# Optimization experiments

Hardware: AMD Instinct MI355X
Metric: run time of the kernel (lower is better)

The kernel has to match this reference:

```python
import jax, jax.numpy as jnp
import numpy as np

B, T, C, H = 4, 2048, 1024, 16
D = C // H  # head_dim = 64

def setup_inputs() -> dict:
    key = jax.random.key(0)
    k1, k2, k3 = jax.random.split(key, 3)
    x = jax.random.normal(k1, (B, T, C), dtype=jnp.float32)
    W_attn = jax.random.normal(k2, (C, 3 * C), dtype=jnp.float32) * (C ** -0.5)
    b_attn = jnp.zeros((3 * C,), dtype=jnp.float32)
    W_proj = jax.random.normal(k3, (C, C), dtype=jnp.float32) * (C ** -0.5)
    b_proj = jnp.zeros((C,), dtype=jnp.float32)
    return {"x": x, "W_attn": W_attn, "b_attn": b_attn, "W_proj": W_proj, "b_proj": b_proj}

def reference(x, W_attn, b_attn, W_proj, b_proj):
    Bc, Tc, Cc = x.shape
    qkv = x @ W_attn + b_attn                       # [B,T,3C]
    q, k, v = jnp.split(qkv, 3, axis=-1)
    q = q.reshape(Bc, Tc, H, D).transpose(0, 2, 1, 3)  # [B,H,T,D]
    k = k.reshape(Bc, Tc, H, D).transpose(0, 2, 1, 3)
    v = v.reshape(Bc, Tc, H, D).transpose(0, 2, 1, 3)
    scores = jnp.einsum('bhqd,bhkd->bhqk', q, k) / jnp.sqrt(jnp.float32(D))
    causal = jnp.tril(jnp.ones((Tc, Tc), dtype=bool))
    scores = jnp.where(causal[None, None, :, :], scores, jnp.float32(-jnp.inf))
    wei = jax.nn.softmax(scores, axis=-1)           # dropout=0 -> identity
    out = jnp.einsum('bhqk,bhkd->bhqd', wei, v)     # [B,H,T,D]
    out = out.transpose(0, 2, 1, 3).reshape(Bc, Tc, Cc)
    return out @ W_proj + b_proj
```

## Files before the change

kernel.cpp:

```cpp
#include <hip/hip_runtime.h>
#include <cstdint>
#include <cstddef>

#define Bsz   4
#define Tsz   2048
#define Csz   1024
#define Hn    16
#define Dh    64
#define Mrows 8192
#define KD    1024

#define NEG_BIG (-1.0e30f)
#define SCL2  0.18033688011112042f
#define PBIAS (-11.541560327111707f)

typedef unsigned short u16;
typedef __bf16  bf16x8 __attribute__((ext_vector_type(8)));
typedef __bf16  bf16x2 __attribute__((ext_vector_type(2)));
typedef float   f32x4  __attribute__((ext_vector_type(4)));
typedef unsigned int u32x4 __attribute__((ext_vector_type(4)));

__device__ __forceinline__ u16 f2bf(float f) {
  union { float f; unsigned int i; } v; v.f = f;
  unsigned int u = v.i;
  return (u16)((u + 0x7fffu + ((u >> 16) & 1u)) >> 16);
}
__device__ __forceinline__ unsigned int pack2bf(float a, float b) {
#if __has_builtin(__builtin_amdgcn_cvt_pk_bf16_f32)
  union { bf16x2 h; unsigned int u; } cv;
  cv.h = __builtin_amdgcn_cvt_pk_bf16_f32(a, b);
  return cv.u;
#else
  return (unsigned int)f2bf(a) | ((unsigned int)f2bf(b) << 16);
#endif
}
__device__ __forceinline__ unsigned int pack2bf_trunc(float lo, float hi) {
  return __builtin_amdgcn_perm(__builtin_bit_cast(unsigned int, hi),
                               __builtin_bit_cast(unsigned int, lo),
                               0x07060302u);
}
__device__ __forceinline__ float fast_exp2(float x) {
#if __has_builtin(__builtin_amdgcn_exp2f)
  return __builtin_amdgcn_exp2f(x);
#else
  return exp2f(x);
#endif
}

__global__ __launch_bounds__(256)
void cvt_f32_bf16(const float* __restrict__ in, u16* __restrict__ out, int n4) {
  const int i = blockIdx.x * 256 + threadIdx.x;
  if (i >= n4) return;
  const float4 v = ((const float4*)in)[i];
  uint2 o;
  o.x = pack2bf(v.x, v.y);
  o.y = pack2bf(v.z, v.w);
  ((uint2*)out)[i] = o;
}

__global__ __launch_bounds__(256)
void transpose_f32_bf16(const float* __restrict__ in, u16* __restrict__ out,
                        int rows, int cols) {
  __shared__ u16 tile[64][65];
  const int tc = blockIdx.x * 64, tr = blockIdx.y * 64;
  const int x = threadIdx.x & 63, y0 = threadIdx.x >> 6;
#pragma unroll
  for (int yy = 0; yy < 64; yy += 4) {
    int r = yy + y0;
    tile[r][x] = f2bf(in[(size_t)(tr + r) * cols + tc + x]);
  }
  __syncthreads();
#pragma unroll
  for (int yy = 0; yy < 64; yy += 4) {
    int r = yy + y0;
    out[(size_t)(tc + r) * rows + tr + x] = tile[x][r];
  }
}

template<int MODE>
__global__ __launch_bounds__(256)
void gemm_bt(const u16* __restrict__ A, const u16* __restrict__ BT,
             const float* __restrict__ bias, u16* __restrict__ o0,
             u16* __restrict__ o1, u16* __restrict__ o2,
             float* __restrict__ fout, int N) {
  __shared__ u16 lsA[128 * 32];
  __shared__ u16 lsB[128 * 32];
  const int tid  = threadIdx.x;
  const int lane = tid & 63;
  const int wid  = tid >> 6;
  const int wm   = wid & 1, wn = wid >> 1;
  const int quad = lane >> 4, l15 = lane & 15;
  const int m0 = blockIdx.y * 128, n0 = blockIdx.x * 128;

  f32x4 acc[4][4];
#pragma unroll
  for (int i = 0; i < 4; ++i)
#pragma unroll
    for (int j = 0; j < 4; ++j) acc[i][j] = (f32x4){0.f, 0.f, 0.f, 0.f};

#if __has_builtin(__builtin_amdgcn_global_load_lds)
  const int srow = lane >> 2, schunk = lane & 3;
  const u16* gA = A  + (size_t)(m0 + wid * 32 + srow) * KD + schunk * 8;
  const u16* gB = BT + (size_t)(n0 + wid * 32 + srow) * KD + schunk * 8;
  u16* lA0 = &lsA[(wid * 32) * 32];
  u16* lB0 = &lsB[(wid * 32) * 32];
#endif

  for (int kk = 0; kk < KD; kk += 32) {
#if __has_builtin(__builtin_amdgcn_global_load_lds)
#pragma unroll
    for (int i = 0; i < 2; ++i) {
      __builtin_amdgcn_global_load_lds(
          (const __attribute__((address_space(1))) void*)(gA + (size_t)i * 16 * KD + kk),
          (__attribute__((address_space(3))) void*)(lA0 + i * 16 * 32), 16, 0, 0);
      __builtin_amdgcn_global_load_lds(
          (const __attribute__((address_space(1))) void*)(gB + (size_t)i * 16 * KD + kk),
          (__attribute__((address_space(3))) void*)(lB0 + i * 16 * 32), 16, 0, 0);
    }
#else
#pragma unroll
    for (int cc = 0; cc < 2; ++cc) {
      int c = tid + cc * 256;
      int row = c >> 2, ch = c & 3;
      *(uint4*)&lsA[row * 32 + ch * 8] =
          *(const uint4*)&A[(size_t)(m0 + row) * KD + kk + ch * 8];
      *(uint4*)&lsB[row * 32 + ch * 8] =
          *(const uint4*)&BT[(size_t)(n0 + row) * KD + kk + ch * 8];
    }
#endif
    __syncthreads();
    bf16x8 af[4], bfv[4];
#pragma unroll
    for (int i = 0; i < 4; ++i)
      af[i] = *(const bf16x8*)&lsA[(wm * 64 + i * 16 + l15) * 32 + quad * 8];
#pragma unroll
    for (int j = 0; j < 4; ++j)
      bfv[j] = *(const bf16x8*)&lsB[(wn * 64 + j * 16 + l15) * 32 + quad * 8];
#pragma unroll
    for (int i = 0; i < 4; ++i)
#pragma unroll
      for (int j = 0; j < 4; ++j)
        acc[i][j] = __builtin_amdgcn_mfma_f32_16x16x32_bf16(af[i], bfv[j],
                                                            acc[i][j], 0, 0, 0);
    __syncthreads();
  }

#pragma unroll
  for (int i = 0; i < 4; ++i) {
#pragma unroll
    for (int j = 0; j < 4; ++j) {
      const int colb = n0 + wn * 64 + j * 16 + l15;
      const float bv = bias[colb];
      float vals[4];
#pragma unroll
      for (int r = 0; r < 4; ++r) vals[r] = acc[i][j][r] + bv;
      const int row0 = m0 + wm * 64 + i * 16 + quad * 4;
      if (MODE == 0) {
        const int b = row0 >> 11, t0 = row0 & (Tsz - 1);
        const int region = colb >> 10;
        const int nc = colb & (Csz - 1);
        const int h = nc >> 6, d = nc & 63;
        if (region == 2) {
          uint2 st;
          st.x = pack2bf(vals[0], vals[1]);
          st.y = pack2bf(vals[2], vals[3]);
          *(uint2*)&o2[((size_t)((b << 4) + h) * Dh + d) * Tsz + t0] = st;
        } else {
          u16* dst = (region == 0) ? o0 : o1;
#pragma unroll
          for (int r = 0; r < 4; ++r)
            dst[(size_t)(((b << 4) + h) * Tsz + t0 + r) * Dh + d] = f2bf(vals[r]);
        }
      } else {
#pragma unroll
        for (int r = 0; r < 4; ++r)
          fout[(size_t)(row0 + r) * N + colb] = vals[r];
      }
    }
  }
}

__global__ __launch_bounds__(128, 4)
void attn_fused(const u16* __restrict__ qb, const u16* __restrict__ kbuf,
                const u16* __restrict__ vT, u16* __restrict__ outp) {
  __shared__ u16 Kl[64 * 72];
  __shared__ u16 Vt[64 * 72];
  const int tid = threadIdx.x, lane = tid & 63, w = tid >> 6;
  const int quad = lane >> 4, l15 = lane & 15;
  const int bh = blockIdx.x;
  const int jq = 31 - blockIdx.y;
  const int b = bh >> 4, h = bh & 15;
  const u16* Q   = qb   + (size_t)bh * Tsz * Dh;
  const u16* Kg  = kbuf + (size_t)bh * Tsz * Dh;
  const u16* VTg = vT   + (size_t)bh * Dh * Tsz;

  const int qrowA = jq * 64 + w * 32 + l15;
  const int qrowB = qrowA + 16;
  const bf16x8 bqA0 = *(const bf16x8*)&Q[(size_t)qrowA * Dh + quad * 8];
  const bf16x8 bqA1 = *(const bf16x8*)&Q[(size_t)qrowA * Dh + 32 + quad * 8];
  const bf16x8 bqB0 = *(const bf16x8*)&Q[(size_t)qrowB * Dh + quad * 8];
  const bf16x8 bqB1 = *(const bf16x8*)&Q[(size_t)qrowB * Dh + 32 + quad * 8];

  f32x4 OA[4], OB[4];
#pragma unroll
  for (int nb = 0; nb < 4; ++nb) {
    OA[nb] = (f32x4){0.f, 0.f, 0.f, 0.f};
    OB[nb] = (f32x4){0.f, 0.f, 0.f, 0.f};
  }
  float lA = 0.f, lB = 0.f;

  for (int j = 0; j <= jq; ++j) {
    const int kb = j * 64;
#pragma unroll
    for (int cc = 0; cc < 4; ++cc) {
      const int c = tid + cc * 128;
      const int rr = c >> 3, off = c & 7;
      *(uint4*)&Kl[rr * 72 + off * 8] =
          *(const uint4*)&Kg[(size_t)(kb + rr) * Dh + off * 8];
      const uint4 vv = *(const uint4*)&VTg[(size_t)rr * Tsz + kb + off * 8];
      const int g0 = off * 2, g1 = off * 2 + 1;
      uint2 st0; st0.x = vv.x; st0.y = vv.y;
      uint2 st1; st1.x = vv.z; st1.y = vv.w;
      *(uint2*)&Vt[rr * 72 + ((g0 >> 3) * 32 + (g0 & 3) * 8 + ((g0 >> 2) & 1) * 4)] = st0;
      *(uint2*)&Vt[rr * 72 + ((g1 >> 3) * 32 + (g1 & 3) * 8 + ((g1 >> 2) & 1) * 4)] = st1;
    }
    __syncthreads();

    const bool diag = (j == jq);
    const int tmaxA = diag ? (2 * w + 1) : 4;
    const int tmaxB = diag ? (2 * w + 2) : 4;

    f32x4 SA[4], SB[4];
#pragma unroll
    for (int t = 0; t < 4; ++t) {
      SA[t] = (f32x4){0.f, 0.f, 0.f, 0.f};
      SB[t] = (f32x4){0.f, 0.f, 0.f, 0.f};
    }
#pragma unroll
    for (int t = 0; t < 4; ++t) {
      if (t < tmaxB) {
        const bf16x8 ak0 = *(const bf16x8*)&Kl[(t * 16 + l15) * 72 + quad * 8];
        const bf16x8 ak1 = *(const bf16x8*)&Kl[(t * 16 + l15) * 72 + 32 + quad * 8];
        if (t < tmaxA) {
          SA[t] = __builtin_amdgcn_mfma_f32_16x16x32_bf16(ak0, bqA0, SA[t], 0, 0, 0);
          SA[t] = __builtin_amdgcn_mfma_f32_16x16x32_bf16(ak1, bqA1, SA[t], 0, 0, 0);
        }
        SB[t] = __builtin_amdgcn_mfma_f32_16x16x32_bf16(ak0, bqB0, SB[t], 0, 0, 0);
        SB[t] = __builtin_amdgcn_mfma_f32_16x16x32_bf16(ak1, bqB1, SB[t], 0, 0, 0);
      }
    }

    float pA[4][4], pB[4][4];
    if (diag) {
#pragma unroll
      for (int t = 0; t < 4; ++t) {
        const int key0 = kb + t * 16 + quad * 4;
#pragma unroll
        for (int r = 0; r < 4; ++r) {
          if (t < tmaxA) {
            const float sv = (key0 + r <= qrowA) ? SA[t][r] : NEG_BIG;
            pA[t][r] = fast_exp2(__builtin_fmaf(sv, SCL2, PBIAS));
            lA += pA[t][r];
          } else pA[t][r] = 0.f;
          if (t < tmaxB) {
            const float sv = (key0 + r <= qrowB) ? SB[t][r] : NEG_BIG;
            pB[t][r] = fast_exp2(__builtin_fmaf(sv, SCL2, PBIAS));
            lB += pB[t][r];
          } else pB[t][r] = 0.f;
        }
      }
    } else {
#pragma unroll
      for (int t = 0; t < 4; ++t)
#pragma unroll
        for (int r = 0; r < 4; ++r) {
          pA[t][r] = fast_exp2(__builtin_fmaf(SA[t][r], SCL2, PBIAS));
          lA += pA[t][r];
          pB[t][r] = fast_exp2(__builtin_fmaf(SB[t][r], SCL2, PBIAS));
          lB += pB[t][r];
        }
    }

    {
      u32x4 puA, puB;
      puA[0] = pack2bf_trunc(pA[0][0], pA[0][1]);
      puA[1] = pack2bf_trunc(pA[0][2], pA[0][3]);
      puA[2] = pack2bf_trunc(pA[1][0], pA[1][1]);
      puA[3] = pack2bf_trunc(pA[1][2], pA[1][3]);
      puB[0] = pack2bf_trunc(pB[0][0], pB[0][1]);
      puB[1] = pack2bf_trunc(pB[0][2], pB[0][3]);
      puB[2] = pack2bf_trunc(pB[1][0], pB[1][1]);
      puB[3] = pack2bf_trunc(pB[1][2], pB[1][3]);
      const bf16x8 pbA = __builtin_bit_cast(bf16x8, puA);
      const bf16x8 pbB = __builtin_bit_cast(bf16x8, puB);
#pragma unroll
      for (int nb = 0; nb < 4; ++nb) {
        const bf16x8 av = *(const bf16x8*)&Vt[(nb * 16 + l15) * 72 + quad * 8];
        OA[nb] = __builtin_amdgcn_mfma_f32_16x16x32_bf16(av, pbA, OA[nb], 0, 0, 0);
        OB[nb] = __builtin_amdgcn_mfma_f32_16x16x32_bf16(av, pbB, OB[nb], 0, 0, 0);
      }
    }
    if (tmaxB > 2) {
      u32x4 puA, puB;
      puA[0] = pack2bf_trunc(pA[2][0], pA[2][1]);
      puA[1] = pack2bf_trunc(pA[2][2], pA[2][3]);
      puA[2] = pack2bf_trunc(pA[3][0], pA[3][1]);
      puA[3] = pack2bf_trunc(pA[3][2], pA[3][3]);
      puB[0] = pack2bf_trunc(pB[2][0], pB[2][1]);
      puB[1] = pack2bf_trunc(pB[2][2], pB[2][3]);
      puB[2] = pack2bf_trunc(pB[3][0], pB[3][1]);
      puB[3] = pack2bf_trunc(pB[3][2], pB[3][3]);
      const bf16x8 pbA = __builtin_bit_cast(bf16x8, puA);
      const bf16x8 pbB = __builtin_bit_cast(bf16x8, puB);
#pragma unroll
      for (int nb = 0; nb < 4; ++nb) {
        const bf16x8 av = *(const bf16x8*)&Vt[(nb * 16 + l15) * 72 + 32 + quad * 8];
        OA[nb] = __builtin_amdgcn_mfma_f32_16x16x32_bf16(av, pbA, OA[nb], 0, 0, 0);
        OB[nb] = __builtin_amdgcn_mfma_f32_16x16x32_bf16(av, pbB, OB[nb], 0, 0, 0);
      }
    }
    __syncthreads();
  }

  float ltA = lA + __shfl_xor(lA, 16, 64);
  ltA += __shfl_xor(ltA, 32, 64);
  float ltB = lB + __shfl_xor(lB, 16, 64);
  ltB += __shfl_xor(ltB, 32, 64);
  const float invA = 1.0f / ltA, invB = 1.0f / ltB;
#pragma unroll
  for (int nb = 0; nb < 4; ++nb) {
    uint2 st;
    st.x = pack2bf(OA[nb][0] * invA, OA[nb][1] * invA);
    st.y = pack2bf(OA[nb][2] * invA, OA[nb][3] * invA);
    *(uint2*)&outp[(size_t)(b * Tsz + qrowA) * Csz + h * Dh + nb * 16 + quad * 4] = st;
    st.x = pack2bf(OB[nb][0] * invB, OB[nb][1] * invB);
    st.y = pack2bf(OB[nb][2] * invB, OB[nb][3] * invB);
    *(uint2*)&outp[(size_t)(b * Tsz + qrowB) * Csz + h * Dh + nb * 16 + quad * 4] = st;
  }
}

extern "C" void kernel_launch(void* const* d_in, const int* in_sizes, int n_in,
                              void* d_out, int out_size, void* d_ws, size_t ws_size,
                              hipStream_t stream) {
  const float* x      = (const float*)d_in[0];
  const float* W_attn = (const float*)d_in[1];
  const float* b_attn = (const float*)d_in[2];
  const float* W_proj = (const float*)d_in[3];
  const float* b_proj = (const float*)d_in[4];
  float* out = (float*)d_out;

  u16* ws   = (u16*)d_ws;
  u16* xbf  = ws;
  u16* qbuf = xbf  + (size_t)Mrows * Csz;
  u16* kbuf = qbuf + (size_t)Mrows * Csz;
  u16* vbuf = kbuf + (size_t)Mrows * Csz;
  u16* aout = vbuf + (size_t)Mrows * Csz;
  u16* WTa  = aout + (size_t)Mrows * Csz;
  u16* WTp  = WTa  + (size_t)Csz * 3 * Csz;

  cvt_f32_bf16<<<(Mrows * Csz / 4 + 255) / 256, 256, 0, stream>>>(
      x, xbf, Mrows * Csz / 4);
  transpose_f32_bf16<<<dim3(3 * Csz / 64, Csz / 64), 256, 0, stream>>>(
      W_attn, WTa, Csz, 3 * Csz);
  transpose_f32_bf16<<<dim3(Csz / 64, Csz / 64), 256, 0, stream>>>(
      W_proj, WTp, Csz, Csz);
  gemm_bt<0><<<dim3(3 * Csz / 128, Mrows / 128), 256, 0, stream>>>(
      xbf, WTa, b_attn, qbuf, kbuf, vbuf, nullptr, 3 * Csz);
  attn_fused<<<dim3(Bsz * Hn, Tsz / 64), 128, 0, stream>>>(
      qbuf, kbuf, vbuf, aout);
  gemm_bt<1><<<dim3(Csz / 128, Mrows / 128), 256, 0, stream>>>(
      aout, WTp, b_proj, nullptr, nullptr, nullptr, out, Csz);
}
```

Measured before the change: 290.4 us.

## Pair causal query blocks per workgroup with 128-row tiles and 4 waves

The attention kernel now uses 256-thread workgroups covering 128 query rows each. Every workgroup handles two query blocks, one from the heavy end and one from the light end of the causal triangle, so all workgroups do about the same work. Each 64-key K/V tile loaded into shared memory is reused by four waves instead of two, cutting global loads per query row. In exchange the grid shrinks to 512 workgroups, occupancy drops to 2 per CU by launch bounds, and the diagonal tiles now need generalized masking logic per wave.

```diff
diff --git a/kernel.cpp b/kernel.cpp
--- a/kernel.cpp
+++ b/kernel.cpp
@@ -180,162 +180,163 @@
   }
 }
 
-__global__ __launch_bounds__(128, 4)
-void attn_fused(const u16* __restrict__ qb, const u16* __restrict__ kbuf,
+__global__ __launch_bounds__(256, 2)
+void attn_fused(const u16* __restrict__ qb_, const u16* __restrict__ kbuf,
                 const u16* __restrict__ vT, u16* __restrict__ outp) {
   __shared__ u16 Kl[64 * 72];
   __shared__ u16 Vt[64 * 72];
   const int tid = threadIdx.x, lane = tid & 63, w = tid >> 6;
   const int quad = lane >> 4, l15 = lane & 15;
   const int bh = blockIdx.x;
-  const int jq = 31 - blockIdx.y;
   const int b = bh >> 4, h = bh & 15;
-  const u16* Q   = qb   + (size_t)bh * Tsz * Dh;
+  const u16* Q   = qb_  + (size_t)bh * Tsz * Dh;
   const u16* Kg  = kbuf + (size_t)bh * Tsz * Dh;
   const u16* VTg = vT   + (size_t)bh * Dh * Tsz;
 
-  const int qrowA = jq * 64 + w * 32 + l15;
-  const int qrowB = qrowA + 16;
-  const bf16x8 bqA0 = *(const bf16x8*)&Q[(size_t)qrowA * Dh + quad * 8];
-  const bf16x8 bqA1 = *(const bf16x8*)&Q[(size_t)qrowA * Dh + 32 + quad * 8];
-  const bf16x8 bqB0 = *(const bf16x8*)&Q[(size_t)qrowB * Dh + quad * 8];
-  const bf16x8 bqB1 = *(const bf16x8*)&Q[(size_t)qrowB * Dh + 32 + quad * 8];
-
-  f32x4 OA[4], OB[4];
-#pragma unroll
-  for (int nb = 0; nb < 4; ++nb) {
-    OA[nb] = (f32x4){0.f, 0.f, 0.f, 0.f};
-    OB[nb] = (f32x4){0.f, 0.f, 0.f, 0.f};
-  }
-  float lA = 0.f, lB = 0.f;
-
-  for (int j = 0; j <= jq; ++j) {
-    const int kb = j * 64;
-#pragma unroll
-    for (int cc = 0; cc < 4; ++cc) {
-      const int c = tid + cc * 128;
-      const int rr = c >> 3, off = c & 7;
-      *(uint4*)&Kl[rr * 72 + off * 8] =
-          *(const uint4*)&Kg[(size_t)(kb + rr) * Dh + off * 8];
-      const uint4 vv = *(const uint4*)&VTg[(size_t)rr * Tsz + kb + off * 8];
-      const int g0 = off * 2, g1 = off * 2 + 1;
-      uint2 st0; st0.x = vv.x; st0.y = vv.y;
-      uint2 st1; st1.x = vv.z; st1.y = vv.w;
-      *(uint2*)&Vt[rr * 72 + ((g0 >> 3) * 32 + (g0 & 3) * 8 + ((g0 >> 2) & 1) * 4)] = st0;
-      *(uint2*)&Vt[rr * 72 + ((g1 >> 3) * 32 + (g1 & 3) * 8 + ((g1 >> 2) & 1) * 4)] = st1;
-    }
-    __syncthreads();
-
-    const bool diag = (j == jq);
-    const int tmaxA = diag ? (2 * w + 1) : 4;
-    const int tmaxB = diag ? (2 * w + 2) : 4;
-
-    f32x4 SA[4], SB[4];
-#pragma unroll
-    for (int t = 0; t < 4; ++t) {
-      SA[t] = (f32x4){0.f, 0.f, 0.f, 0.f};
-      SB[t] = (f32x4){0.f, 0.f, 0.f, 0.f};
-    }
-#pragma unroll
-    for (int t = 0; t < 4; ++t) {
-      if (t < tmaxB) {
-        const bf16x8 ak0 = *(const bf16x8*)&Kl[(t * 16 + l15) * 72 + quad * 8];
-        const bf16x8 ak1 = *(const bf16x8*)&Kl[(t * 16 + l15) * 72 + 32 + quad * 8];
-        if (t < tmaxA) {
-          SA[t] = __builtin_amdgcn_mfma_f32_16x16x32_bf16(ak0, bqA0, SA[t], 0, 0, 0);
-          SA[t] = __builtin_amdgcn_mfma_f32_16x16x32_bf16(ak1, bqA1, SA[t], 0, 0, 0);
-        }
-        SB[t] = __builtin_amdgcn_mfma_f32_16x16x32_bf16(ak0, bqB0, SB[t], 0, 0, 0);
-        SB[t] = __builtin_amdgcn_mfma_f32_16x16x32_bf16(ak1, bqB1, SB[t], 0, 0, 0);
+  for (int ph = 0; ph < 2; ++ph) {
+    const int qb = ph ? (int)blockIdx.y : 15 - (int)blockIdx.y;
+    const int qbase = qb * 128 + w * 32;
+    const int qrowA = qbase + l15, qrowB = qrowA + 16;
+
+    const bf16x8 bqA0 = *(const bf16x8*)&Q[(size_t)qrowA * Dh + quad * 8];
+    const bf16x8 bqA1 = *(const bf16x8*)&Q[(size_t)qrowA * Dh + 32 + quad * 8];
+    const bf16x8 bqB0 = *(const bf16x8*)&Q[(size_t)qrowB * Dh + quad * 8];
+    const bf16x8 bqB1 = *(const bf16x8*)&Q[(size_t)qrowB * Dh + 32 + quad * 8];
+
+    f32x4 OA[4], OB[4];
+#pragma unroll
+    for (int nb = 0; nb < 4; ++nb) {
+      OA[nb] = (f32x4){0.f, 0.f, 0.f, 0.f};
+      OB[nb] = (f32x4){0.f, 0.f, 0.f, 0.f};
+    }
+    float lA = 0.f, lB = 0.f;
+
+    const int jmax = 2 * qb + 1;
+    for (int j = 0; j <= jmax; ++j) {
+      const int kb = j * 64;
+#pragma unroll
+      for (int cc = 0; cc < 2; ++cc) {
+        const int c = tid + cc * 256;
+        const int rr = c >> 3, off = c & 7;
+        *(uint4*)&Kl[rr * 72 + off * 8] =
+            *(const uint4*)&Kg[(size_t)(kb + rr) * Dh + off * 8];
+        const uint4 vv = *(const uint4*)&VTg[(size_t)rr * Tsz + kb + off * 8];
+        const int g0 = off * 2, g1 = off * 2 + 1;
+        uint2 st0; st0.x = vv.x; st0.y = vv.y;
+        uint2 st1; st1.x = vv.z; st1.y = vv.w;
+        *(uint2*)&Vt[rr * 72 + ((g0 >> 3) * 32 + (g0 & 3) * 8 + ((g0 >> 2) & 1) * 4)] = st0;
+        *(uint2*)&Vt[rr * 72 + ((g1 >> 3) * 32 + (g1 & 3) * 8 + ((g1 >> 2) & 1) * 4)] = st1;
       }
-    }
-
-    float pA[4][4], pB[4][4];
-    if (diag) {
-#pragma unroll
-      for (int t = 0; t < 4; ++t) {
-        const int key0 = kb + t * 16 + quad * 4;
-#pragma unroll
-        for (int r = 0; r < 4; ++r) {
-          if (t < tmaxA) {
-            const float sv = (key0 + r <= qrowA) ? SA[t][r] : NEG_BIG;
-            pA[t][r] = fast_exp2(__builtin_fmaf(sv, SCL2, PBIAS));
-            lA += pA[t][r];
-          } else pA[t][r] = 0.f;
+      __syncthreads();
+
+      const int db = qbase - kb;
+      const int t4 = db >> 4;
+      const int tmaxA = min(4, max(0, t4 + 1));
+      const int tmaxB = min(4, max(0, t4 + 2));
+      const bool maskA = db < 64;
+      const bool maskB = db < 48;
+
+      if (tmaxB > 0) {
+        f32x4 SA[4], SB[4];
+#pragma unroll
+        for (int t = 0; t < 4; ++t) {
+          SA[t] = (f32x4){0.f, 0.f, 0.f, 0.f};
+          SB[t] = (f32x4){0.f, 0.f, 0.f, 0.f};
+        }
+#pragma unroll
+        for (int t = 0; t < 4; ++t) {
           if (t < tmaxB) {
-            const float sv = (key0 + r <= qrowB) ? SB[t][r] : NEG_BIG;
-            pB[t][r] = fast_exp2(__builtin_fmaf(sv, SCL2, PBIAS));
-            lB += pB[t][r];
-          } else pB[t][r] = 0.f;
+            const bf16x8 ak0 = *(const bf16x8*)&Kl[(t * 16 + l15) * 72 + quad * 8];
+            const bf16x8 ak1 = *(const bf16x8*)&Kl[(t * 16 + l15) * 72 + 32 + quad * 8];
+            if (t < tmaxA) {
+              SA[t] = __builtin_amdgcn_mfma_f32_16x16x32_bf16(ak0, bqA0, SA[t], 0, 0, 0);
+              SA[t] = __builtin_amdgcn_mfma_f32_16x16x32_bf16(ak1, bqA1, SA[t], 0, 0, 0);
+            }
+            SB[t] = __builtin_amdgcn_mfma_f32_16x16x32_bf16(ak0, bqB0, SB[t], 0, 0, 0);
+            SB[t] = __builtin_amdgcn_mfma_f32_16x16x32_bf16(ak1, bqB1, SB[t], 0, 0, 0);
+          }
+        }
+
+        float pA[4][4], pB[4][4];
+#pragma unroll
+        for (int t = 0; t < 4; ++t) {
+          const int key0 = kb + t * 16 + quad * 4;
+#pragma unroll
+          for (int r = 0; r < 4; ++r) {
+            if (t < tmaxA) {
+              const float sv =
+                  (!maskA || key0 + r <= qrowA) ? SA[t][r] : NEG_BIG;
+              pA[t][r] = fast_exp2(__builtin_fmaf(sv, SCL2, PBIAS));
+              lA += pA[t][r];
+            } else pA[t][r] = 0.f;
+            if (t < tmaxB) {
+              const float sv =
+                  (!maskB || key0 + r <= qrowB) ? SB[t][r] : NEG_BIG;
+              pB[t][r] = fast_exp2(__builtin_fmaf(sv, SCL2, PBIAS));
+              lB += pB[t][r];
+            } else pB[t][r] = 0.f;
+          }
+        }
+
+        {
+          u32x4 puA, puB;
+          puA[0] = pack2bf_trunc(pA[0][0], pA[0][1]);
+          puA[1] = pack2bf_trunc(pA[0][2], pA[0][3]);
+          puA[2] = pack2bf_trunc(pA[1][0], pA[1][1]);
+          puA[3] = pack2bf_trunc(pA[1][2], pA[1][3]);
+          puB[0] = pack2bf_trunc(pB[0][0], pB[0][1]);
+          puB[1] = pack2bf_trunc(pB[0][2], pB[0][3]);
+          puB[2] = pack2bf_trunc(pB[1][0], pB[1][1]);
+          puB[3] = pack2bf_trunc(pB[1][2], pB[1][3]);
+          const bf16x8 pbA = __builtin_bit_cast(bf16x8, puA);
+          const bf16x8 pbB = __builtin_bit_cast(bf16x8, puB);
+#pragma unroll
+          for (int nb = 0; nb < 4; ++nb) {
+            const bf16x8 av = *(const bf16x8*)&Vt[(nb * 16 + l15) * 72 + quad * 8];
+            if (tmaxA > 0)
+              OA[nb] = __builtin_amdgcn_mfma_f32_16x16x32_bf16(av, pbA, OA[nb], 0, 0, 0);
+            OB[nb] = __builtin_amdgcn_mfma_f32_16x16x32_bf16(av, pbB, OB[nb], 0, 0, 0);
+          }
+        }
+        if (tmaxB > 2) {
+          u32x4 puA, puB;
+          puA[0] = pack2bf_trunc(pA[2][0], pA[2][1]);
+          puA[1] = pack2bf_trunc(pA[2][2], pA[2][3]);
+          puA[2] = pack2bf_trunc(pA[3][0], pA[3][1]);
+          puA[3] = pack2bf_trunc(pA[3][2], pA[3][3]);
+          puB[0] = pack2bf_trunc(pB[2][0], pB[2][1]);
+          puB[1] = pack2bf_trunc(pB[2][2], pB[2][3]);
+          puB[2] = pack2bf_trunc(pB[3][0], pB[3][1]);
+          puB[3] = pack2bf_trunc(pB[3][2], pB[3][3]);
+          const bf16x8 pbA = __builtin_bit_cast(bf16x8, puA);
+          const bf16x8 pbB = __builtin_bit_cast(bf16x8, puB);
+#pragma unroll
+          for (int nb = 0; nb < 4; ++nb) {
+            const bf16x8 av = *(const bf16x8*)&Vt[(nb * 16 + l15) * 72 + 32 + quad * 8];
+            if (tmaxA > 2)
+              OA[nb] = __builtin_amdgcn_mfma_f32_16x16x32_bf16(av, pbA, OA[nb], 0, 0, 0);
+            OB[nb] = __builtin_amdgcn_mfma_f32_16x16x32_bf16(av, pbB, OB[nb], 0, 0, 0);
+          }
         }
       }
-    } else {
-#pragma unroll
-      for (int t = 0; t < 4; ++t)
-#pragma unroll
-        for (int r = 0; r < 4; ++r) {
-          pA[t][r] = fast_exp2(__builtin_fmaf(SA[t][r], SCL2, PBIAS));
-          lA += pA[t][r];
-          pB[t][r] = fast_exp2(__builtin_fmaf(SB[t][r], SCL2, PBIAS));
-          lB += pB[t][r];
-        }
-    }
-
-    {
-      u32x4 puA, puB;
-      puA[0] = pack2bf_trunc(pA[0][0], pA[0][1]);
-      puA[1] = pack2bf_trunc(pA[0][2], pA[0][3]);
-      puA[2] = pack2bf_trunc(pA[1][0], pA[1][1]);
-      puA[3] = pack2bf_trunc(pA[1][2], pA[1][3]);
-      puB[0] = pack2bf_trunc(pB[0][0], pB[0][1]);
-      puB[1] = pack2bf_trunc(pB[0][2], pB[0][3]);
-      puB[2] = pack2bf_trunc(pB[1][0], pB[1][1]);
-      puB[3] = pack2bf_trunc(pB[1][2], pB[1][3]);
-      const bf16x8 pbA = __builtin_bit_cast(bf16x8, puA);
-      const bf16x8 pbB = __builtin_bit_cast(bf16x8, puB);
-#pragma unroll
-      for (int nb = 0; nb < 4; ++nb) {
-        const bf16x8 av = *(const bf16x8*)&Vt[(nb * 16 + l15) * 72 + quad * 8];
-        OA[nb] = __builtin_amdgcn_mfma_f32_16x16x32_bf16(av, pbA, OA[nb], 0, 0, 0);
-        OB[nb] = __builtin_amdgcn_mfma_f32_16x16x32_bf16(av, pbB, OB[nb], 0, 0, 0);
-      }
-    }
-    if (tmaxB > 2) {
-      u32x4 puA, puB;
-      puA[0] = pack2bf_trunc(pA[2][0], pA[2][1]);
-      puA[1] = pack2bf_trunc(pA[2][2], pA[2][3]);
-      puA[2] = pack2bf_trunc(pA[3][0], pA[3][1]);
-      puA[3] = pack2bf_trunc(pA[3][2], pA[3][3]);
-      puB[0] = pack2bf_trunc(pB[2][0], pB[2][1]);
-      puB[1] = pack2bf_trunc(pB[2][2], pB[2][3]);
-      puB[2] = pack2bf_trunc(pB[3][0], pB[3][1]);
-      puB[3] = pack2bf_trunc(pB[3][2], pB[3][3]);
-      const bf16x8 pbA = __builtin_bit_cast(bf16x8, puA);
-      const bf16x8 pbB = __builtin_bit_cast(bf16x8, puB);
-#pragma unroll
-      for (int nb = 0; nb < 4; ++nb) {
-        const bf16x8 av = *(const bf16x8*)&Vt[(nb * 16 + l15) * 72 + 32 + quad * 8];
-        OA[nb] = __builtin_amdgcn_mfma_f32_16x16x32_bf16(av, pbA, OA[nb], 0, 0, 0);
-        OB[nb] = __builtin_amdgcn_mfma_f32_16x16x32_bf16(av, pbB, OB[nb], 0, 0, 0);
-      }
-    }
-    __syncthreads();
-  }
-
-  float ltA = lA + __shfl_xor(lA, 16, 64);
-  ltA += __shfl_xor(ltA, 32, 64);
-  float ltB = lB + __shfl_xor(lB, 16, 64);
-  ltB += __shfl_xor(ltB, 32, 64);
-  const float invA = 1.0f / ltA, invB = 1.0f / ltB;
-#pragma unroll
-  for (int nb = 0; nb < 4; ++nb) {
-    uint2 st;
-    st.x = pack2bf(OA[nb][0] * invA, OA[nb][1] * invA);
-    st.y = pack2bf(OA[nb][2] * invA, OA[nb][3] * invA);
-    *(uint2*)&outp[(size_t)(b * Tsz + qrowA) * Csz + h * Dh + nb * 16 + quad * 4] = st;
-    st.x = pack2bf(OB[nb][0] * invB, OB[nb][1] * invB);
-    st.y = pack2bf(OB[nb][2] * invB, OB[nb][3] * invB);
-    *(uint2*)&outp[(size_t)(b * Tsz + qrowB) * Csz + h * Dh + nb * 16 + quad * 4] = st;
+      __syncthreads();
+    }
+
+    float ltA = lA + __shfl_xor(lA, 16, 64);
+    ltA += __shfl_xor(ltA, 32, 64);
+    float ltB = lB + __shfl_xor(lB, 16, 64);
+    ltB += __shfl_xor(ltB, 32, 64);
+    const float invA = 1.0f / ltA, invB = 1.0f / ltB;
+#pragma unroll
+    for (int nb = 0; nb < 4; ++nb) {
+      uint2 st;
+      st.x = pack2bf(OA[nb][0] * invA, OA[nb][1] * invA);
+      st.y = pack2bf(OA[nb][2] * invA, OA[nb][3] * invA);
+      *(uint2*)&outp[(size_t)(b * Tsz + qrowA) * Csz + h * Dh + nb * 16 + quad * 4] = st;
+      st.x = pack2bf(OB[nb][0] * invB, OB[nb][1] * invB);
+      st.y = pack2bf(OB[nb][2] * invB, OB[nb][3] * invB);
+      *(uint2*)&outp[(size_t)(b * Tsz + qrowB) * Csz + h * Dh + nb * 16 + quad * 4] = st;
+    }
   }
 }
 
@@ -366,7 +367,7 @@
       W_proj, WTp, Csz, Csz);
   gemm_bt<0><<<dim3(3 * Csz / 128, Mrows / 128), 256, 0, stream>>>(
       xbf, WTa, b_attn, qbuf, kbuf, vbuf, nullptr, 3 * Csz);
-  attn_fused<<<dim3(Bsz * Hn, Tsz / 64), 128, 0, stream>>>(
+  attn_fused<<<dim3(Bsz * Hn, 8), 256, 0, stream>>>(
       qbuf, kbuf, vbuf, aout);
   gemm_bt<1><<<dim3(Csz / 128, Mrows / 128), 256, 0, stream>>>(
       aout, WTp, b_proj, nullptr, nullptr, nullptr, out, Csz);
```

After: 291.1 us. About the same (+0.3%).
